# Performance work log

Measured on AMD Instinct MI355X. Metric: run time of the kernel, lower is better.

Reference implementation:

```python
import jax, jax.numpy as jnp
import numpy as np

N_NODES = 50000
N_EDGES = 800000
DIM = 128
LN_EPS = 1e-5


def setup_inputs() -> dict:
    key = jax.random.key(0)
    k1, k2, k3, k4 = jax.random.split(key, 4)
    h = jax.random.normal(k1, (N_NODES, DIM), dtype=jnp.float32)
    edge_index = jax.random.randint(k2, (2, N_EDGES), 0, N_NODES, dtype=jnp.int64)
    W = jax.random.normal(k3, (DIM, DIM), dtype=jnp.float32) / np.sqrt(DIM)
    b = jnp.zeros((DIM,), dtype=jnp.float32)
    gamma = jnp.ones((DIM,), dtype=jnp.float32)
    beta = jnp.zeros((DIM,), dtype=jnp.float32)
    t = jnp.zeros((), dtype=jnp.float32)
    return {"t": t, "h": h, "edge_index": edge_index, "batch_size": N_NODES,
            "W": W, "b": b, "gamma": gamma, "beta": beta}


def _gcn_conv(h, edge_index, W, b):
    """PyG-style GCNConv: D^{-1/2} (A+I) D^{-1/2} (h W) + b."""
    N = h.shape[0]
    loops = jnp.arange(N, dtype=edge_index.dtype)
    src = jnp.concatenate([edge_index[0], loops])  # [E+N]
    dst = jnp.concatenate([edge_index[1], loops])  # [E+N]
    # degree (with self loops) on destination nodes
    deg = jax.ops.segment_sum(jnp.ones_like(dst, dtype=h.dtype), dst, num_segments=N)
    dinv = jnp.where(deg > 0, jax.lax.rsqrt(deg), 0.0)
    norm = dinv[src] * dinv[dst]                    # [E+N]
    xw = h @ W                                      # [N, D]
    msg = xw[src] * norm[:, None]                   # gather + scale, [E+N, D]
    agg = jax.ops.segment_sum(msg, dst, num_segments=N)  # scatter-add, [N, D]
    return agg + b


def reference(t, h, edge_index, batch_size, W, b, gamma, beta):
    if h.ndim == 1:
        h = h[None, :]
    dh = _gcn_conv(h, edge_index, W, b)
    # LayerNorm over feature dim, then tanh
    mean = jnp.mean(dh, axis=-1, keepdims=True)
    var = jnp.mean(jnp.square(dh - mean), axis=-1, keepdims=True)
    dh = (dh - mean) * jax.lax.rsqrt(var + LN_EPS) * gamma + beta
    dh = jnp.tanh(dh)
    return (dh, jnp.zeros_like(edge_index), jnp.zeros_like(jnp.asarray(batch_size)))
```

## Files before the change

kernel.cpp:

```cpp
#include <hip/hip_runtime.h>
#include <math.h>

#define NN 50000
#define NE 800000
#define D  128
#define SCAN_CHUNK 1024
#define NSCAN ((NN + SCAN_CHUNK - 1) / SCAN_CHUNK)
#define PG_BLOCKS 782

typedef __attribute__((ext_vector_type(8))) short bf16x8;
typedef __attribute__((ext_vector_type(4))) float f32x4;

__device__ __forceinline__ unsigned short f32_to_bf16(float f) {
    unsigned u = __float_as_uint(f);
    u = u + 0x7FFFu + ((u >> 16) & 1u);
    return (unsigned short)(u >> 16);
}

__global__ __launch_bounds__(256) void k_prep_gemm(
        const float* __restrict__ h,  const float* __restrict__ Wg,
        const int* __restrict__ ei,   int* __restrict__ deg,
        unsigned short* __restrict__ rank,
        unsigned short* __restrict__ zb,
        int* __restrict__ outtail, int tailN) {
    __shared__ unsigned short Wl[D * D];
    int tid = threadIdx.x;

#pragma unroll 4
    for (int i = 0; i < 64; i++) {
        int e = i * 256 + tid;
        int k = e >> 7, n = e & 127;
        int frag = (n >> 4) * 256 + (k >> 5) * 64 + ((k >> 3) & 3) * 16 + (n & 15);
        Wl[frag * 8 + (k & 7)] = f32_to_bf16(Wg[e]);
    }

    int g = blockIdx.x * 256 + tid;
    if (g < NE / 4) {
        int4 d4 = ((const int4*)(ei + NE))[g];
        ushort4 r;
        r.x = (unsigned short)atomicAdd(&deg[d4.x], 1);
        r.y = (unsigned short)atomicAdd(&deg[d4.y], 1);
        r.z = (unsigned short)atomicAdd(&deg[d4.z], 1);
        r.w = (unsigned short)atomicAdd(&deg[d4.w], 1);
        ((ushort4*)rank)[g] = r;
    }
    for (int i = g; i < tailN; i += PG_BLOCKS * 256) outtail[i] = 0;

    int w = tid >> 6, lane = tid & 63;
    int quad = lane >> 4, lo = lane & 15;
    int rowBase = blockIdx.x * 64 + w * 16;
    int rowA = rowBase + lo; if (rowA > NN - 1) rowA = NN - 1;
    const float4* h4 = (const float4*)h;

    bf16x8 af[4];
#pragma unroll
    for (int kt = 0; kt < 4; kt++) {
        float4 u = h4[(size_t)rowA * 32 + kt * 8 + quad * 2];
        float4 v = h4[(size_t)rowA * 32 + kt * 8 + quad * 2 + 1];
        bf16x8 a;
        a[0] = (short)f32_to_bf16(u.x); a[1] = (short)f32_to_bf16(u.y);
        a[2] = (short)f32_to_bf16(u.z); a[3] = (short)f32_to_bf16(u.w);
        a[4] = (short)f32_to_bf16(v.x); a[5] = (short)f32_to_bf16(v.y);
        a[6] = (short)f32_to_bf16(v.z); a[7] = (short)f32_to_bf16(v.w);
        af[kt] = a;
    }
    __syncthreads();

    f32x4 acc[8];
#pragma unroll
    for (int nt = 0; nt < 8; nt++) acc[nt] = (f32x4){0.f, 0.f, 0.f, 0.f};

    const uint4* Wl4 = (const uint4*)Wl;
#pragma unroll
    for (int kt = 0; kt < 4; kt++) {
#pragma unroll
        for (int nt = 0; nt < 8; nt++) {
            uint4 tb = Wl4[nt * 256 + kt * 64 + lane];
            bf16x8 bfv = __builtin_bit_cast(bf16x8, tb);
            acc[nt] = __builtin_amdgcn_mfma_f32_16x16x32_bf16(af[kt], bfv, acc[nt], 0, 0, 0);
        }
    }

#pragma unroll
    for (int reg = 0; reg < 4; reg++) {
        int row = rowBase + quad * 4 + reg;
        if (row < NN) {
#pragma unroll
            for (int nt = 0; nt < 8; nt++)
                zb[(size_t)row * D + nt * 16 + lo] = f32_to_bf16(acc[nt][reg]);
        }
    }
}

__global__ __launch_bounds__(256) void k_scan(const int* __restrict__ deg,
                                              int* __restrict__ partial,
                                              int* __restrict__ flag,
                                              int* __restrict__ rowoff,
                                              float* __restrict__ dinv) {
    __shared__ int sbuf[256];
    int t = threadIdx.x;
    int bid = blockIdx.x;
    int base = bid * SCAN_CHUNK + t * 4;
    int d[4]; int s = 0;
#pragma unroll
    for (int j = 0; j < 4; j++) {
        int i = base + j;
        d[j] = 0;
        if (i < NN) {
            d[j] = deg[i];
            s += d[j];
            dinv[i] = rsqrtf((float)d[j] + 1.0f);
        }
    }
    sbuf[t] = s; __syncthreads();
    for (int off = 1; off < 256; off <<= 1) {
        int v = (t >= off) ? sbuf[t - off] : 0;
        __syncthreads();
        sbuf[t] += v;
        __syncthreads();
    }
    if (t == 0) {
        atomicExch(&partial[bid], sbuf[255]);
        __threadfence();
        atomicAdd(flag, 1);
        while (atomicAdd(flag, 0) < NSCAN) {}
    }
    __syncthreads();

    int lane = t & 63;
    int pv = (lane < NSCAN && lane < bid) ? atomicAdd(&partial[lane], 0) : 0;
#pragma unroll
    for (int off = 32; off > 0; off >>= 1) pv += __shfl_xor(pv, off, 64);

    int ex = sbuf[t] - s + pv;
#pragma unroll
    for (int j = 0; j < 4; j++) {
        int i = base + j;
        if (i < NN) {
            rowoff[i] = ex;
            ex += d[j];
            if (i == NN - 1) rowoff[NN] = ex;
        }
    }
}

__global__ __launch_bounds__(320) void k_fill(const int* __restrict__ ei,
                                              const int* __restrict__ rowoff,
                                              const unsigned short* __restrict__ rank,
                                              int* __restrict__ csr) {
    int t = blockIdx.x * 320 + threadIdx.x;
    int4 s4 = ((const int4*)ei)[t];
    int4 d4 = ((const int4*)(ei + NE))[t];
    ushort4 r4 = ((const ushort4*)rank)[t];
    csr[rowoff[d4.x] + r4.x] = s4.x;
    csr[rowoff[d4.y] + r4.y] = s4.y;
    csr[rowoff[d4.z] + r4.z] = s4.z;
    csr[rowoff[d4.w] + r4.w] = s4.w;
}

__global__ __launch_bounds__(256) void k_gather_ln(
        const int* __restrict__ rowoff, const int* __restrict__ csr,
        const float* __restrict__ dinv, const unsigned* __restrict__ zbu,
        const float* __restrict__ bias, const float* __restrict__ gamma,
        const float* __restrict__ beta, float* __restrict__ out) {
    int tid = threadIdx.x;
    int w = tid >> 6, lane = tid & 63;
    int rowBase = blockIdx.x * 16 + w * 4;

    float2 x[4];
    for (int r = 0; r < 4; r++) {
        int row = rowBase + r;
        float dn = dinv[row];
        unsigned zr = zbu[(size_t)row * 64 + lane];
        float2 a;
        a.x = dn * __uint_as_float(zr << 16);
        a.y = dn * __uint_as_float(zr & 0xFFFF0000u);
        int start = rowoff[row], end = rowoff[row + 1];
        for (int c = start; c < end; c += 64) {
            int m = end - c; if (m > 64) m = 64;
            int s = 0; float wv = 0.f;
            if (lane < m) { s = csr[c + lane]; wv = dinv[s]; }
            int j = 0;
            for (; j + 7 < m; j += 8) {
                unsigned p[8]; float wj[8];
#pragma unroll
                for (int q = 0; q < 8; q++) {
                    int sq = __shfl(s, j + q, 64);
                    wj[q]  = __shfl(wv, j + q, 64);
                    p[q]   = zbu[(size_t)sq * 64 + lane];
                }
#pragma unroll
                for (int q = 0; q < 8; q++) {
                    a.x = fmaf(wj[q], __uint_as_float(p[q] << 16), a.x);
                    a.y = fmaf(wj[q], __uint_as_float(p[q] & 0xFFFF0000u), a.y);
                }
            }
            for (; j < m; j++) {
                int   sj = __shfl(s,  j, 64);
                float fj = __shfl(wv, j, 64);
                unsigned pj = zbu[(size_t)sj * 64 + lane];
                a.x = fmaf(fj, __uint_as_float(pj << 16), a.x);
                a.y = fmaf(fj, __uint_as_float(pj & 0xFFFF0000u), a.y);
            }
        }
        a.x *= dn; a.y *= dn;
        x[r] = a;
    }

    float2 bi = ((const float2*)bias)[lane];
    float2 ga = ((const float2*)gamma)[lane];
    float2 be = ((const float2*)beta)[lane];
#pragma unroll
    for (int r = 0; r < 4; r++) {
        int row = rowBase + r;
        float y0 = x[r].x + bi.x;
        float y1 = x[r].y + bi.y;
        float s = y0 + y1;
#pragma unroll
        for (int off = 32; off > 0; off >>= 1) s += __shfl_xor(s, off, 64);
        float m = s * (1.0f / 128.0f);
        float v0 = y0 - m, v1 = y1 - m;
        float vs = v0 * v0 + v1 * v1;
#pragma unroll
        for (int off = 32; off > 0; off >>= 1) vs += __shfl_xor(vs, off, 64);
        float rstd = rsqrtf(vs * (1.0f / 128.0f) + 1e-5f);
        float2 o;
        o.x = tanhf(v0 * rstd * ga.x + be.x);
        o.y = tanhf(v1 * rstd * ga.y + be.y);
        *(float2*)&out[(size_t)row * D + lane * 2] = o;
    }
}

extern "C" void kernel_launch(void* const* d_in, const int* in_sizes, int n_in,
                              void* d_out, int out_size, void* d_ws, size_t ws_size,
                              hipStream_t stream) {
    const float* h     = (const float*)d_in[1];
    const int*   ei    = (const int*)  d_in[2];
    const float* Wg    = (const float*)d_in[4];
    const float* b     = (const float*)d_in[5];
    const float* gamma = (const float*)d_in[6];
    const float* beta  = (const float*)d_in[7];
    float* out = (float*)d_out;

    int*            deg    = (int*)d_ws;
    int*            flag   = deg + NN;
    int*            partial= flag + 1;
    unsigned short* rank   = (unsigned short*)(partial + 64);
    int*            rowoff = (int*)(rank + NE);
    float*          dinv   = (float*)(rowoff + NN + 1);
    int*            csr    = (int*)(dinv + NN);
    unsigned short* zb     = (unsigned short*)(csr + NE);

    int tailN = out_size - NN * D;
    int* outtail = (int*)(out + (size_t)NN * D);

    hipMemsetAsync(deg, 0, (NN + 1) * sizeof(int), stream);
    k_prep_gemm<<<PG_BLOCKS, 256, 0, stream>>>(h, Wg, ei, deg, rank, zb, outtail, tailN);
    k_scan     <<<NSCAN,     256, 0, stream>>>(deg, partial, flag, rowoff, dinv);
    k_fill     <<<625,       320, 0, stream>>>(ei, rowoff, rank, csr);
    k_gather_ln<<<NN / 16,   256, 0, stream>>>(rowoff, csr, dinv, (const unsigned*)zb, b, gamma, beta, out);
}
```

Before: 206.5 us.

## Prescale GEMM rows by dinv, pack W once, fuse GEMM with CSR fill

The GEMM moves from the degree-count kernel into the CSR-fill kernel. Each row of hW is multiplied by dinv[row] before the bf16 store, so the gather no longer loads per-edge dinv or does weighted FMAs and becomes a plain sum. W is packed into MFMA fragment order once by block 0 into workspace, instead of every block converting it into LDS. The gather loop now reads 8 CSR indices uniformly and pads with a zeroed sentinel row NN, which removes the shuffles. The costs are an extra pass over padded loads and a dependency of the GEMM on the scan output, since the GEMM can no longer overlap the degree count.

```diff
diff --git a/kernel.cpp b/kernel.cpp
--- a/kernel.cpp
+++ b/kernel.cpp
@@ -17,24 +17,14 @@
     return (unsigned short)(u >> 16);
 }
 
-__global__ __launch_bounds__(256) void k_prep_gemm(
-        const float* __restrict__ h,  const float* __restrict__ Wg,
-        const int* __restrict__ ei,   int* __restrict__ deg,
-        unsigned short* __restrict__ rank,
-        unsigned short* __restrict__ zb,
+__global__ __launch_bounds__(256) void k_count(
+        const float* __restrict__ Wg, const int* __restrict__ ei,
+        int* __restrict__ deg, unsigned short* __restrict__ rank,
+        unsigned short* __restrict__ wpk, unsigned short* __restrict__ zb,
         int* __restrict__ outtail, int tailN) {
-    __shared__ unsigned short Wl[D * D];
     int tid = threadIdx.x;
-
-#pragma unroll 4
-    for (int i = 0; i < 64; i++) {
-        int e = i * 256 + tid;
-        int k = e >> 7, n = e & 127;
-        int frag = (n >> 4) * 256 + (k >> 5) * 64 + ((k >> 3) & 3) * 16 + (n & 15);
-        Wl[frag * 8 + (k & 7)] = f32_to_bf16(Wg[e]);
-    }
-
     int g = blockIdx.x * 256 + tid;
+
     if (g < NE / 4) {
         int4 d4 = ((const int4*)(ei + NE))[g];
         ushort4 r;
@@ -46,50 +36,19 @@
     }
     for (int i = g; i < tailN; i += PG_BLOCKS * 256) outtail[i] = 0;
 
-    int w = tid >> 6, lane = tid & 63;
-    int quad = lane >> 4, lo = lane & 15;
-    int rowBase = blockIdx.x * 64 + w * 16;
-    int rowA = rowBase + lo; if (rowA > NN - 1) rowA = NN - 1;
-    const float4* h4 = (const float4*)h;
-
-    bf16x8 af[4];
-#pragma unroll
-    for (int kt = 0; kt < 4; kt++) {
-        float4 u = h4[(size_t)rowA * 32 + kt * 8 + quad * 2];
-        float4 v = h4[(size_t)rowA * 32 + kt * 8 + quad * 2 + 1];
-        bf16x8 a;
-        a[0] = (short)f32_to_bf16(u.x); a[1] = (short)f32_to_bf16(u.y);
-        a[2] = (short)f32_to_bf16(u.z); a[3] = (short)f32_to_bf16(u.w);
-        a[4] = (short)f32_to_bf16(v.x); a[5] = (short)f32_to_bf16(v.y);
-        a[6] = (short)f32_to_bf16(v.z); a[7] = (short)f32_to_bf16(v.w);
-        af[kt] = a;
-    }
-    __syncthreads();
-
-    f32x4 acc[8];
-#pragma unroll
-    for (int nt = 0; nt < 8; nt++) acc[nt] = (f32x4){0.f, 0.f, 0.f, 0.f};
-
-    const uint4* Wl4 = (const uint4*)Wl;
-#pragma unroll
-    for (int kt = 0; kt < 4; kt++) {
-#pragma unroll
-        for (int nt = 0; nt < 8; nt++) {
-            uint4 tb = Wl4[nt * 256 + kt * 64 + lane];
-            bf16x8 bfv = __builtin_bit_cast(bf16x8, tb);
-            acc[nt] = __builtin_amdgcn_mfma_f32_16x16x32_bf16(af[kt], bfv, acc[nt], 0, 0, 0);
-        }
-    }
-
-#pragma unroll
-    for (int reg = 0; reg < 4; reg++) {
-        int row = rowBase + quad * 4 + reg;
-        if (row < NN) {
-#pragma unroll
-            for (int nt = 0; nt < 8; nt++)
-                zb[(size_t)row * D + nt * 16 + lo] = f32_to_bf16(acc[nt][reg]);
-        }
-    }
+    if (blockIdx.x == 0) {
+#pragma unroll 8
+        for (int i = 0; i < 64; i++) {
+            int o = i * 256 + tid;
+            int j = o & 7, frag = o >> 3;
+            int lo = frag & 15, quad = (frag >> 4) & 3;
+            int kt = (frag >> 6) & 3, nt = frag >> 8;
+            int k = kt * 32 + quad * 8 + j, n = nt * 16 + lo;
+            wpk[o] = f32_to_bf16(Wg[k * 128 + n]);
+        }
+    }
+    if (blockIdx.x == 1 && tid < 64)
+        ((unsigned*)(zb + (size_t)NN * D))[tid] = 0u;
 }
 
 __global__ __launch_bounds__(256) void k_scan(const int* __restrict__ deg,
@@ -144,18 +103,67 @@
     }
 }
 
-__global__ __launch_bounds__(320) void k_fill(const int* __restrict__ ei,
-                                              const int* __restrict__ rowoff,
-                                              const unsigned short* __restrict__ rank,
-                                              int* __restrict__ csr) {
-    int t = blockIdx.x * 320 + threadIdx.x;
-    int4 s4 = ((const int4*)ei)[t];
-    int4 d4 = ((const int4*)(ei + NE))[t];
-    ushort4 r4 = ((const ushort4*)rank)[t];
-    csr[rowoff[d4.x] + r4.x] = s4.x;
-    csr[rowoff[d4.y] + r4.y] = s4.y;
-    csr[rowoff[d4.z] + r4.z] = s4.z;
-    csr[rowoff[d4.w] + r4.w] = s4.w;
+__global__ __launch_bounds__(256) void k_gemm_fill(
+        const float* __restrict__ h, const uint4* __restrict__ wpk4,
+        const int* __restrict__ ei, const unsigned short* __restrict__ rank,
+        const int* __restrict__ rowoff, const float* __restrict__ dinv,
+        unsigned short* __restrict__ zb, int* __restrict__ csr) {
+    int tid = threadIdx.x;
+    int g = blockIdx.x * 256 + tid;
+
+    if (g < NE / 4) {
+        int4 s4 = ((const int4*)ei)[g];
+        int4 d4 = ((const int4*)(ei + NE))[g];
+        ushort4 r4 = ((const ushort4*)rank)[g];
+        csr[rowoff[d4.x] + r4.x] = s4.x;
+        csr[rowoff[d4.y] + r4.y] = s4.y;
+        csr[rowoff[d4.z] + r4.z] = s4.z;
+        csr[rowoff[d4.w] + r4.w] = s4.w;
+    }
+
+    int w = tid >> 6, lane = tid & 63;
+    int quad = lane >> 4, lo = lane & 15;
+    int rowBase = blockIdx.x * 64 + w * 16;
+    int rowA = rowBase + lo; if (rowA > NN - 1) rowA = NN - 1;
+    const float4* h4 = (const float4*)h;
+
+    bf16x8 af[4];
+#pragma unroll
+    for (int kt = 0; kt < 4; kt++) {
+        float4 u = h4[(size_t)rowA * 32 + kt * 8 + quad * 2];
+        float4 v = h4[(size_t)rowA * 32 + kt * 8 + quad * 2 + 1];
+        bf16x8 a;
+        a[0] = (short)f32_to_bf16(u.x); a[1] = (short)f32_to_bf16(u.y);
+        a[2] = (short)f32_to_bf16(u.z); a[3] = (short)f32_to_bf16(u.w);
+        a[4] = (short)f32_to_bf16(v.x); a[5] = (short)f32_to_bf16(v.y);
+        a[6] = (short)f32_to_bf16(v.z); a[7] = (short)f32_to_bf16(v.w);
+        af[kt] = a;
+    }
+
+    f32x4 acc[8];
+#pragma unroll
+    for (int nt = 0; nt < 8; nt++) acc[nt] = (f32x4){0.f, 0.f, 0.f, 0.f};
+
+#pragma unroll
+    for (int kt = 0; kt < 4; kt++) {
+#pragma unroll
+        for (int nt = 0; nt < 8; nt++) {
+            uint4 tb = wpk4[nt * 256 + kt * 64 + lane];
+            bf16x8 bfv = __builtin_bit_cast(bf16x8, tb);
+            acc[nt] = __builtin_amdgcn_mfma_f32_16x16x32_bf16(af[kt], bfv, acc[nt], 0, 0, 0);
+        }
+    }
+
+#pragma unroll
+    for (int reg = 0; reg < 4; reg++) {
+        int row = rowBase + quad * 4 + reg;
+        if (row < NN) {
+            float dn = dinv[row];
+#pragma unroll
+            for (int nt = 0; nt < 8; nt++)
+                zb[(size_t)row * D + nt * 16 + lo] = f32_to_bf16(acc[nt][reg] * dn);
+        }
+    }
 }
 
 __global__ __launch_bounds__(256) void k_gather_ln(
@@ -168,39 +176,32 @@
     int rowBase = blockIdx.x * 16 + w * 4;
 
     float2 x[4];
+#pragma unroll
     for (int r = 0; r < 4; r++) {
-        int row = rowBase + r;
+        int row = __builtin_amdgcn_readfirstlane(rowBase + r);
         float dn = dinv[row];
         unsigned zr = zbu[(size_t)row * 64 + lane];
         float2 a;
-        a.x = dn * __uint_as_float(zr << 16);
-        a.y = dn * __uint_as_float(zr & 0xFFFF0000u);
-        int start = rowoff[row], end = rowoff[row + 1];
-        for (int c = start; c < end; c += 64) {
-            int m = end - c; if (m > 64) m = 64;
-            int s = 0; float wv = 0.f;
-            if (lane < m) { s = csr[c + lane]; wv = dinv[s]; }
-            int j = 0;
-            for (; j + 7 < m; j += 8) {
-                unsigned p[8]; float wj[8];
-#pragma unroll
-                for (int q = 0; q < 8; q++) {
-                    int sq = __shfl(s, j + q, 64);
-                    wj[q]  = __shfl(wv, j + q, 64);
-                    p[q]   = zbu[(size_t)sq * 64 + lane];
-                }
-#pragma unroll
-                for (int q = 0; q < 8; q++) {
-                    a.x = fmaf(wj[q], __uint_as_float(p[q] << 16), a.x);
-                    a.y = fmaf(wj[q], __uint_as_float(p[q] & 0xFFFF0000u), a.y);
-                }
+        a.x = __uint_as_float(zr << 16);
+        a.y = __uint_as_float(zr & 0xFFFF0000u);
+        int cs = __builtin_amdgcn_readfirstlane(rowoff[row]);
+        int ce = __builtin_amdgcn_readfirstlane(rowoff[row + 1]);
+        for (int c = cs; c < ce; c += 8) {
+            int m = ce - c;
+            int s[8];
+#pragma unroll
+            for (int q = 0; q < 8; q++) {
+                int t = csr[c + q];
+                s[q] = (q < m) ? t : NN;
             }
-            for (; j < m; j++) {
-                int   sj = __shfl(s,  j, 64);
-                float fj = __shfl(wv, j, 64);
-                unsigned pj = zbu[(size_t)sj * 64 + lane];
-                a.x = fmaf(fj, __uint_as_float(pj << 16), a.x);
-                a.y = fmaf(fj, __uint_as_float(pj & 0xFFFF0000u), a.y);
+            unsigned p[8];
+#pragma unroll
+            for (int q = 0; q < 8; q++)
+                p[q] = zbu[(size_t)s[q] * 64 + lane];
+#pragma unroll
+            for (int q = 0; q < 8; q++) {
+                a.x += __uint_as_float(p[q] << 16);
+                a.y += __uint_as_float(p[q] & 0xFFFF0000u);
             }
         }
         a.x *= dn; a.y *= dn;
@@ -242,21 +243,23 @@
     const float* beta  = (const float*)d_in[7];
     float* out = (float*)d_out;
 
-    int*            deg    = (int*)d_ws;
-    int*            flag   = deg + NN;
-    int*            partial= flag + 1;
-    unsigned short* rank   = (unsigned short*)(partial + 64);
-    int*            rowoff = (int*)(rank + NE);
-    float*          dinv   = (float*)(rowoff + NN + 1);
-    int*            csr    = (int*)(dinv + NN);
-    unsigned short* zb     = (unsigned short*)(csr + NE);
+    char* wsb = (char*)d_ws;
+    unsigned short* wpk    = (unsigned short*)(wsb);
+    int*            deg    = (int*)(wsb + 32768);
+    int*            flag   = (int*)(wsb + 232768);
+    int*            partial= (int*)(wsb + 232832);
+    unsigned short* rank   = (unsigned short*)(wsb + 233088);
+    int*            rowoff = (int*)(wsb + 1833088);
+    float*          dinv   = (float*)(wsb + 2633152);
+    int*            csr    = (int*)(wsb + 2833152);
+    unsigned short* zb     = (unsigned short*)(wsb + 6033152);
 
     int tailN = out_size - NN * D;
     int* outtail = (int*)(out + (size_t)NN * D);
 
-    hipMemsetAsync(deg, 0, (NN + 1) * sizeof(int), stream);
-    k_prep_gemm<<<PG_BLOCKS, 256, 0, stream>>>(h, Wg, ei, deg, rank, zb, outtail, tailN);
+    hipMemsetAsync(deg, 0, NN * sizeof(int) + sizeof(int), stream);
+    k_count    <<<PG_BLOCKS, 256, 0, stream>>>(Wg, ei, deg, rank, wpk, zb, outtail, tailN);
     k_scan     <<<NSCAN,     256, 0, stream>>>(deg, partial, flag, rowoff, dinv);
-    k_fill     <<<625,       320, 0, stream>>>(ei, rowoff, rank, csr);
+    k_gemm_fill<<<PG_BLOCKS, 256, 0, stream>>>(h, (const uint4*)wpk, ei, rank, rowoff, dinv, zb, csr);
     k_gather_ln<<<NN / 16,   256, 0, stream>>>(rowoff, csr, dinv, (const unsigned*)zb, b, gamma, beta, out);
 }
```

Result: faster. 196.1 us (-5.1%).
